# Performance work log

Measured on AMD Instinct MI355X. Metric: run time of the kernel, lower is better.

The kernel has to match this reference:

```python
import jax, jax.numpy as jnp
import numpy as np

B, S, DIM = 2, 2048, 2048
H, KVH, HD = 16, 4, 128
G = H // KVH  # GQA groups = 4
THETA = 10000.0


def setup_inputs() -> dict:
    key = jax.random.key(0)
    k0, k1, k2, k3, k4 = jax.random.split(key, 5)
    x = jax.random.normal(k0, (B, S, DIM), jnp.float32)
    # RoPE table: [max_seq_len, head_dim//2, 2] holding (cos, sin)
    inv_freq = 1.0 / (THETA ** (jnp.arange(0, HD, 2, dtype=jnp.float32) / HD))
    angles = jnp.outer(jnp.arange(S, dtype=jnp.float32), inv_freq)  # [S, HD//2]
    freqs_cis = jnp.stack([jnp.cos(angles), jnp.sin(angles)], axis=-1)
    sc = 0.02
    wq = jax.random.normal(k1, (H * HD, DIM), jnp.float32) * sc
    wk = jax.random.normal(k2, (KVH * HD, DIM), jnp.float32) * sc
    wv = jax.random.normal(k3, (KVH * HD, DIM), jnp.float32) * sc
    wo = jax.random.normal(k4, (DIM, H * HD), jnp.float32) * sc
    return {"x": x, "freqs_cis": freqs_cis, "wq": wq, "wk": wk, "wv": wv, "wo": wo}


def apply_rope(x, freqs_cis):
    # x: [B, S, h, HD]; freqs_cis: [max_S, HD//2, 2]
    s = x.shape[1]
    xr = x.astype(jnp.float32).reshape(*x.shape[:-1], -1, 2)  # [B,S,h,HD//2,2]
    cos = freqs_cis[:s, :, 0][None, :, None, :]  # [1,S,1,HD//2]
    sin = freqs_cis[:s, :, 1][None, :, None, :]
    x0, x1 = xr[..., 0], xr[..., 1]
    out = jnp.stack([x0 * cos - x1 * sin, x0 * sin + x1 * cos], axis=-1)
    return out.reshape(x.shape).astype(x.dtype)


def reference(x, freqs_cis, wq, wk, wv, wo):
    b, s, d = x.shape
    q = (x @ wq.T).reshape(b, s, H, HD)
    k = (x @ wk.T).reshape(b, s, KVH, HD)
    v = (x @ wv.T).reshape(b, s, KVH, HD)
    q = apply_rope(q, freqs_cis)
    k = apply_rope(k, freqs_cis)
    # GQA expand: repeat_interleave along head dim
    k = jnp.repeat(k, G, axis=2)  # [b,s,H,HD]
    v = jnp.repeat(v, G, axis=2)
    q = jnp.swapaxes(q, 1, 2)  # [b,H,s,HD]
    k = jnp.swapaxes(k, 1, 2)
    v = jnp.swapaxes(v, 1, 2)
    scale = 1.0 / jnp.sqrt(jnp.asarray(HD, dtype=q.dtype))
    scores = jnp.einsum('bhqd,bhkd->bhqk', q, k) * scale  # [b,H,s,s]
    causal = jnp.tril(jnp.ones((s, s), dtype=bool))
    scores = jnp.where(causal[None, None], scores, jnp.finfo(scores.dtype).min)
    probs = jax.nn.softmax(scores, axis=-1)
    attn = jnp.einsum('bhqk,bhkd->bhqd', probs, v)  # [b,H,s,HD]
    attn = jnp.swapaxes(attn, 1, 2).reshape(b, s, H * HD)
    return attn @ wo.T
```

## Files before the change

kernel.cpp:

```cpp
#include <hip/hip_runtime.h>
#include <stdint.h>

#define B_ 2
#define S_ 2048
#define DIM_ 2048
#define H_ 16
#define KVH_ 4
#define HD_ 128

typedef short short8 __attribute__((ext_vector_type(8)));
typedef float f4 __attribute__((ext_vector_type(4)));
typedef float f16v __attribute__((ext_vector_type(16)));
typedef unsigned int uint2v __attribute__((ext_vector_type(2)));
typedef unsigned short u16;

#define KSCALE (0.08838834764831845f * 1.4426950408889634f)

__device__ __forceinline__ float bf2f(u16 u) {
    union { unsigned int i; float f; } c; c.i = ((unsigned int)u) << 16; return c.f;
}
__device__ __forceinline__ u16 f2bf(float f) {
    union { float f; unsigned int i; } c; c.f = f;
    return (u16)((c.i + 0x7fffu + ((c.i >> 16) & 1u)) >> 16);
}
__device__ __forceinline__ unsigned pk_bf16(float lo, float hi) {
    unsigned r;
    asm("v_cvt_pk_bf16_f32 %0, %1, %2" : "=v"(r) : "v"(lo), "v"(hi));
    return r;
}

#define GLDS16(gp, lp) \
    __builtin_amdgcn_global_load_lds((const __attribute__((address_space(1))) unsigned int*)(gp), \
                                     (__attribute__((address_space(3))) unsigned int*)(lp), 16, 0, 0)

#define BAR()     asm volatile("s_barrier" ::: "memory")
#define WAITLGKM() asm volatile("s_waitcnt lgkmcnt(0)" ::: "memory")

__global__ void cast_all(const float* __restrict__ x,  const float* __restrict__ wq,
                         const float* __restrict__ wk, const float* __restrict__ wv,
                         const float* __restrict__ wo,
                         u16* __restrict__ xb, u16* __restrict__ wqkvb, u16* __restrict__ wob) {
    int i = blockIdx.x * 256 + threadIdx.x;
    const float4* src; ushort4* dst; int j;
    if (i < 2097152)      { src = (const float4*)x;  dst = (ushort4*)xb;                 j = i; }
    else if (i < 3145728) { src = (const float4*)wq; dst = (ushort4*)wqkvb;              j = i - 2097152; }
    else if (i < 3407872) { src = (const float4*)wk; dst = (ushort4*)wqkvb + 1048576;    j = i - 3145728; }
    else if (i < 3670016) { src = (const float4*)wv; dst = (ushort4*)wqkvb + 1310720;    j = i - 3407872; }
    else                  { src = (const float4*)wo; dst = (ushort4*)wob;                j = i - 3670016; }
    float4 v = src[j];
    ushort4 o;
    o.x = f2bf(v.x); o.y = f2bf(v.y); o.z = f2bf(v.z); o.w = f2bf(v.w);
    dst[j] = o;
}

template<bool OUT_BF16, int NBX>
__global__ __launch_bounds__(512, 2) void gemm256(const u16* __restrict__ A,
                                                  const u16* __restrict__ W,
                                                  void* __restrict__ Cout,
                                                  int M, int N, int K) {
    __shared__ u16 As[2][16384];
    __shared__ u16 Bs[2][16384];
    int t = threadIdx.x, lane = t & 63, w = t >> 6;
    int quad = lane >> 4, l16 = lane & 15, l7 = lane & 7;
    int wm = w >> 2, wn = w & 3;
    int bid = blockIdx.x;
    int xcd = bid & 7, grp = bid >> 3;
    int bx = grp % NBX, by = (grp / NBX) * 8 + xcd;
    size_t m0 = (size_t)by * 256, n0 = (size_t)bx * 256;

    int srow = lane >> 3;
    int sunit = (lane & 7) ^ srow;
    int rR0a = (w >> 2) * 64 + (w & 3) * 8;
    const u16* Ag = A + (m0 + srow) * (size_t)K + sunit * 8;
    const u16* Bg = W + (n0 + srow) * (size_t)K + sunit * 8;

#define STG_A(pl, tk, r0) GLDS16(Ag + ((size_t)((r0) + w * 8)) * K + (tk) * 64, (pl) + ((r0) + w * 8) * 64)
#define STG_B(pl, tk, r0) GLDS16(Bg + ((size_t)((r0) + w * 8)) * K + (tk) * 64, (pl) + ((r0) + w * 8) * 64)
#define STG_BR(pl, tk, bse) GLDS16(Bg + ((size_t)((bse) + rR0a)) * K + (tk) * 64, (pl) + ((bse) + rR0a) * 64)

#define LDA(mh) { \
    _Pragma("unroll") for (int i_ = 0; i_ < 4; i_++) \
    _Pragma("unroll") for (int k_ = 0; k_ < 2; k_++) \
        a[i_][k_] = *(const short8*)&pAc[(wm * 128 + (mh) * 64 + i_ * 16 + l16) * 64 + (((quad + 4 * k_) ^ l7) << 3)]; }
#define LDB(nh) { \
    _Pragma("unroll") for (int j_ = 0; j_ < 2; j_++) \
    _Pragma("unroll") for (int k_ = 0; k_ < 2; k_++) \
        b[j_][k_] = *(const short8*)&pBc[(wn * 64 + (nh) * 32 + j_ * 16 + l16) * 64 + (((quad + 4 * k_) ^ l7) << 3)]; }
#define MFMA_Q(mh, nh) { \
    __builtin_amdgcn_s_setprio(1); \
    _Pragma("unroll") for (int i_ = 0; i_ < 4; i_++) \
    _Pragma("unroll") for (int j_ = 0; j_ < 2; j_++) \
    _Pragma("unroll") for (int k_ = 0; k_ < 2; k_++) \
        acc[(mh) * 4 + i_][(nh) * 2 + j_] = __builtin_amdgcn_mfma_f32_16x16x32_bf16( \
            a[i_][k_], b[j_][k_], acc[(mh) * 4 + i_][(nh) * 2 + j_], 0, 0, 0); \
    __builtin_amdgcn_s_setprio(0); }

    f4 acc[8][4];
    #pragma unroll
    for (int i = 0; i < 8; i++)
        #pragma unroll
        for (int j = 0; j < 4; j++) acc[i][j] = (f4){0.f, 0.f, 0.f, 0.f};

    int NT = K >> 6;

    #pragma unroll
    for (int pt = 0; pt < 2; pt++) {
        u16* pa = &As[pt][0]; u16* pb = &Bs[pt][0];
        #pragma unroll
        for (int r0 = 0; r0 < 256; r0 += 64) { STG_A(pa, pt, r0); STG_B(pb, pt, r0); }
    }
    asm volatile("s_waitcnt vmcnt(0)" ::: "memory");
    BAR();

    short8 a[4][2], b[2][2];
    for (int tt = 0; tt < NT; tt++) {
        int c = tt & 1, nc = c ^ 1;
        u16* pAc = &As[c][0];  u16* pBc = &Bs[c][0];
        u16* pAn = &As[nc][0]; u16* pBn = &Bs[nc][0];
        bool s1 = (tt >= 1) & (tt + 1 < NT);
        bool s2 = (tt + 2 < NT);
        LDA(0); LDB(0);
        if (s1) { STG_A(pAn, tt + 1, 64); STG_A(pAn, tt + 1, 192); }
        BAR(); WAITLGKM(); MFMA_Q(0, 0); BAR();
        LDB(1);
        if (s1) { STG_BR(pBn, tt + 1, 32); STG_BR(pBn, tt + 1, 160); }
        BAR(); WAITLGKM(); MFMA_Q(0, 1); BAR();
        LDA(1); LDB(0);
        if (s2) { STG_A(pAc, tt + 2, 0); STG_A(pAc, tt + 2, 128); }
        BAR(); WAITLGKM(); MFMA_Q(1, 0); BAR();
        if (s2) asm volatile("s_waitcnt vmcnt(2)" ::: "memory");
        else    asm volatile("s_waitcnt vmcnt(0)" ::: "memory");
        LDB(1);
        if (s2) { STG_BR(pBc, tt + 2, 0); STG_BR(pBc, tt + 2, 128); }
        BAR(); WAITLGKM(); MFMA_Q(1, 1); BAR();
    }

    #pragma unroll
    for (int i = 0; i < 8; i++) {
        size_t row = m0 + wm * 128 + i * 16 + quad * 4;
        #pragma unroll
        for (int j = 0; j < 4; j++) {
            size_t col = n0 + wn * 64 + j * 16 + l16;
            #pragma unroll
            for (int r = 0; r < 4; r++) {
                if (OUT_BF16) ((u16*)Cout)[(row + r) * (size_t)N + col] = f2bf(acc[i][j][r]);
                else          ((float*)Cout)[(row + r) * (size_t)N + col] = acc[i][j][r];
            }
        }
    }
#undef STG_A
#undef STG_B
#undef STG_BR
#undef LDA
#undef LDB
#undef MFMA_Q
}

__global__ __launch_bounds__(256) void pack_k(const u16* __restrict__ QKV,
                                              const float* __restrict__ freqs,
                                              u16* __restrict__ Kp) {
    int gid = blockIdx.x * 256 + threadIdx.x;
    int u = gid & 15, row = (gid >> 4) & 63, kt = (gid >> 10) & 31, bk = gid >> 15;
    int b = bk >> 2, kvh = bk & 3;
    int s = kt * 64 + row;
    int d8 = u ^ (row & 7);
    const u16* src = QKV + (size_t)(b * S_ + s) * 3072 + 2048 + kvh * HD_ + d8 * 8;
    short8 v = *(const short8*)src;
    short8 o;
    #pragma unroll
    for (int jp = 0; jp < 4; jp++) {
        float2 cw = ((const float2*)freqs)[s * 64 + d8 * 4 + jp];
        float x0 = bf2f((u16)v[2 * jp]), x1 = bf2f((u16)v[2 * jp + 1]);
        o[2 * jp]     = (short)f2bf(x0 * cw.x - x1 * cw.y);
        o[2 * jp + 1] = (short)f2bf(x0 * cw.y + x1 * cw.x);
    }
    *(short8*)&Kp[(size_t)gid * 8] = o;
}

__global__ __launch_bounds__(256) void pack_v(const u16* __restrict__ QKV, u16* __restrict__ Vp) {
    __shared__ u16 L[64 * 136];
    int bid = blockIdx.x;
    int bk = bid & 7, kt = bid >> 3;
    int b = bk >> 2, kvh = bk & 3;
    int t = threadIdx.x;
    const u16* src = QKV + (size_t)(b * S_ + kt * 64) * 3072 + 2560 + kvh * HD_;
    #pragma unroll
    for (int it = 0; it < 4; it++) {
        int idx = t + it * 256;
        int r = idx >> 4, c = idx & 15;
        *(short8*)&L[r * 136 + c * 8] = *(const short8*)(src + (size_t)r * 3072 + c * 8);
    }
    __syncthreads();
    u16* dst = Vp + (size_t)(bk * 32 + kt) * 8192;
    #pragma unroll
    for (int it = 0; it < 4; it++) {
        int idx = t + it * 256;
        int hd = idx >> 3, u = idx & 7;
        int k0 = (u ^ (hd & 7)) * 8;
        short8 v;
        #pragma unroll
        for (int jj = 0; jj < 8; jj++) v[jj] = (short)L[(k0 + jj) * 136 + hd];
        *(short8*)&dst[(size_t)idx * 8] = v;
    }
}

__global__ __launch_bounds__(256) __attribute__((amdgpu_waves_per_eu(2, 2)))
void attn_kernel(const u16* __restrict__ QKV,
                 const float* __restrict__ freqs,
                 const u16* __restrict__ Kp,
                 const u16* __restrict__ Vp,
                 u16* __restrict__ Ob) {
    __shared__ u16 Ks[2][8192];
    __shared__ u16 Vs[2][8192];
    int bid = blockIdx.x;
    int jj_ = bid & 255, half = bid >> 8;
    int bk = jj_ & 7, qpr = jj_ >> 3;
    int qb = half ? qpr : 63 - qpr;
    int b = bk >> 2, kvh = bk & 3;
    int t = threadIdx.x, lane = t & 63, w = t >> 6;
    int l31 = lane & 31, hi = lane >> 5, l7 = lane & 7;
    int h = kvh * 4 + w;
    int nkt = (qb >> 1) + 1;

    short8 qf[8];
    {
        int s = qb * 32 + l31;
        const u16* qp = QKV + ((size_t)(b * S_ + s)) * 3072 + h * HD_ + hi * 8;
        const float2* fr2 = (const float2*)freqs;
        #pragma unroll
        for (int ds = 0; ds < 8; ds++) {
            short8 v = *(const short8*)(qp + ds * 16);
            short8 o;
            #pragma unroll
            for (int jp = 0; jp < 4; jp++) {
                float2 cs = fr2[s * 64 + ds * 8 + hi * 4 + jp];
                float x0 = bf2f((u16)v[2 * jp]), x1 = bf2f((u16)v[2 * jp + 1]);
                o[2 * jp]     = (short)f2bf((x0 * cs.x - x1 * cs.y) * KSCALE);
                o[2 * jp + 1] = (short)f2bf((x0 * cs.y + x1 * cs.x) * KSCALE);
            }
            qf[ds] = o;
        }
    }

    float m_i = -3e38f, ls = 0.f;
    f16v o4[4];
    #pragma unroll
    for (int i = 0; i < 4; i++)
        #pragma unroll
        for (int r = 0; r < 16; r++) o4[i][r] = 0.f;

    const u16* Kpb = Kp + (size_t)bk * 32 * 8192;
    const u16* Vpb = Vp + (size_t)bk * 32 * 8192;
    int so = w * 2048 + lane * 8;

    {
        const u16* ks = Kpb + so;
        const u16* vs = Vpb + so;
        #pragma unroll
        for (int i = 0; i < 4; i++) {
            GLDS16(ks + i * 512, &Ks[0][w * 2048 + i * 512]);
            GLDS16(vs + i * 512, &Vs[0][w * 2048 + i * 512]);
        }
    }

    for (int kt = 0; kt < nkt; kt++) {
        int buf = kt & 1;
        __syncthreads();
        if (kt + 1 < nkt) {
            int nb = buf ^ 1;
            const u16* ks = Kpb + (size_t)(kt + 1) * 8192 + so;
            const u16* vs = Vpb + (size_t)(kt + 1) * 8192 + so;
            #pragma unroll
            for (int i = 0; i < 4; i++) {
                GLDS16(ks + i * 512, &Ks[nb][w * 2048 + i * 512]);
                GLDS16(vs + i * 512, &Vs[nb][w * 2048 + i * 512]);
            }
        }

        f16v sacc[2];
        #pragma unroll
        for (int k2 = 0; k2 < 2; k2++)
            #pragma unroll
            for (int r = 0; r < 16; r++) sacc[k2][r] = 0.f;
        __builtin_amdgcn_s_setprio(1);
        #pragma unroll
        for (int ds = 0; ds < 8; ds++) {
            int uK = ((ds * 2 + hi) ^ l7) * 8;
            short8 kf0 = *(const short8*)&Ks[buf][l31 * 128 + uK];
            short8 kf1 = *(const short8*)&Ks[buf][(32 + l31) * 128 + uK];
            sacc[0] = __builtin_amdgcn_mfma_f32_32x32x16_bf16(kf0, qf[ds], sacc[0], 0, 0, 0);
            sacc[1] = __builtin_amdgcn_mfma_f32_32x32x16_bf16(kf1, qf[ds], sacc[1], 0, 0, 0);
        }
        __builtin_amdgcn_s_setprio(0);

        short8 vf[16];
        #pragma unroll
        for (int ks = 0; ks < 4; ks++) {
            int uV = ((ks * 2 + hi) ^ l7) * 8;
            #pragma unroll
            for (int ht = 0; ht < 4; ht++)
                vf[ks * 4 + ht] = *(const short8*)&Vs[buf][(ht * 32 + l31) * 64 + uV];
        }

        if (kt == nkt - 1) {
            int off0 = kt * 64 - qb * 32;
            #pragma unroll
            for (int k2 = 0; k2 < 2; k2++) {
                #pragma unroll
                for (int r = 0; r < 16; r++) {
                    int colo = off0 + k2 * 32 + (r & 3) + ((r >> 2) << 3) + (hi << 2);
                    if (colo > l31) sacc[k2][r] = -3e38f;
                }
            }
        }

        float mx[16];
        #pragma unroll
        for (int r = 0; r < 16; r++) mx[r] = fmaxf(sacc[0][r], sacc[1][r]);
        #pragma unroll
        for (int s_ = 8; s_ > 0; s_ >>= 1)
            #pragma unroll
            for (int r = 0; r < s_; r++) mx[r] = fmaxf(mx[r], mx[r + s_]);
        float pm = fmaxf(mx[0], __shfl_xor(mx[0], 32, 64));
        if (__any(pm > m_i + 8.0f)) {
            float mnew = fmaxf(m_i, pm);
            float al = exp2f(m_i - mnew);
            ls *= al;
            #pragma unroll
            for (int i = 0; i < 4; i++)
                #pragma unroll
                for (int r = 0; r < 16; r++) o4[i][r] *= al;
            m_i = mnew;
        }

        short8 pa[4];
        #pragma unroll
        for (int k2 = 0; k2 < 2; k2++) {
            float p[16];
            #pragma unroll
            for (int r = 0; r < 16; r++) p[r] = exp2f(sacc[k2][r] - m_i);
            float s0 = (p[0] + p[1]) + (p[2] + p[3]);
            float s1 = (p[4] + p[5]) + (p[6] + p[7]);
            float s2 = (p[8] + p[9]) + (p[10] + p[11]);
            float s3 = (p[12] + p[13]) + (p[14] + p[15]);
            ls += (s0 + s1) + (s2 + s3);
            unsigned W0 = pk_bf16(p[0], p[1]),   W1 = pk_bf16(p[2], p[3]);
            unsigned W2 = pk_bf16(p[4], p[5]),   W3 = pk_bf16(p[6], p[7]);
            unsigned W4 = pk_bf16(p[8], p[9]),   W5 = pk_bf16(p[10], p[11]);
            unsigned W6 = pk_bf16(p[12], p[13]), W7 = pk_bf16(p[14], p[15]);
            uint2v r02 = __builtin_amdgcn_permlane32_swap(W0, W2, false, false);
            uint2v r13 = __builtin_amdgcn_permlane32_swap(W1, W3, false, false);
            uint2v r46 = __builtin_amdgcn_permlane32_swap(W4, W6, false, false);
            uint2v r57 = __builtin_amdgcn_permlane32_swap(W5, W7, false, false);
            union { unsigned u[4]; short8 s8; } flo, fhi;
            flo.u[0] = r02[0]; flo.u[1] = r13[0]; flo.u[2] = r02[1]; flo.u[3] = r13[1];
            fhi.u[0] = r46[0]; fhi.u[1] = r57[0]; fhi.u[2] = r46[1]; fhi.u[3] = r57[1];
            pa[k2 * 2]     = flo.s8;
            pa[k2 * 2 + 1] = fhi.s8;
        }

        __builtin_amdgcn_s_setprio(1);
        #pragma unroll
        for (int ks = 0; ks < 4; ks++) {
            #pragma unroll
            for (int ht = 0; ht < 4; ht++)
                o4[ht] = __builtin_amdgcn_mfma_f32_32x32x16_bf16(vf[ks * 4 + ht], pa[ks], o4[ht], 0, 0, 0);
        }
        __builtin_amdgcn_s_setprio(0);
    }

    ls += __shfl_xor(ls, 32, 64);
    float rl = 1.0f / ls;
    size_t row = (size_t)b * S_ + qb * 32 + l31;
    u16* op = Ob + row * 2048 + h * HD_;
    #pragma unroll
    for (int ht = 0; ht < 4; ht++) {
        #pragma unroll
        for (int g = 0; g < 4; g++) {
            ushort4 st;
            st.x = f2bf(o4[ht][4 * g + 0] * rl);
            st.y = f2bf(o4[ht][4 * g + 1] * rl);
            st.z = f2bf(o4[ht][4 * g + 2] * rl);
            st.w = f2bf(o4[ht][4 * g + 3] * rl);
            *(ushort4*)&op[ht * 32 + g * 8 + hi * 4] = st;
        }
    }
}

extern "C" void kernel_launch(void* const* d_in, const int* in_sizes, int n_in,
                              void* d_out, int out_size, void* d_ws, size_t ws_size,
                              hipStream_t stream) {
    const float* x     = (const float*)d_in[0];
    const float* freqs = (const float*)d_in[1];
    const float* wq    = (const float*)d_in[2];
    const float* wk    = (const float*)d_in[3];
    const float* wv    = (const float*)d_in[4];
    const float* wo    = (const float*)d_in[5];
    float* out = (float*)d_out;

    char* p = (char*)d_ws;
    u16* xb    = (u16*)p; p += (size_t)4096 * 2048 * 2;
    u16* wqkvb = (u16*)p; p += (size_t)3072 * 2048 * 2;
    u16* wob   = (u16*)p; p += (size_t)2048 * 2048 * 2;
    u16* QKVb  = (u16*)p; p += (size_t)4096 * 3072 * 2;
    u16* Kpb   = (u16*)p; p += (size_t)8 * 32 * 8192 * 2;
    u16* Vpb   = (u16*)p; p += (size_t)8 * 32 * 8192 * 2;
    u16* attnb = xb;

    cast_all<<<18432, 256, 0, stream>>>(x, wq, wk, wv, wo, xb, wqkvb, wob);

    gemm256<true, 12><<<192, 512, 0, stream>>>(xb, wqkvb, QKVb, 4096, 3072, 2048);

    pack_k<<<1024, 256, 0, stream>>>(QKVb, freqs, Kpb);
    pack_v<<<256, 256, 0, stream>>>(QKVb, Vpb);

    attn_kernel<<<512, 256, 0, stream>>>(QKVb, freqs, Kpb, Vpb, attnb);

    gemm256<false, 8><<<128, 512, 0, stream>>>(attnb, wob, out, 4096, 2048, 2048);
}
```

Measured before the change: 318.0 us.

## Pack K/V in MFMA fragment order and load directly from global per-wave

The K and V packing kernels now write tiles in the exact per-lane MFMA fragment order, so the attention kernel can read its operands with contiguous 16-byte global loads instead of staging through LDS. The attention kernel becomes single-wave blocks (2048 blocks of 64 threads), each handling one head and q-block, with a new causal-balanced block ordering. This removes LDS staging, barriers and the double-buffer logic. In exchange it loses the sharing of K/V tiles across the four GQA heads in one block, relies on L2 for reuse, and has no explicit prefetch of the next tile.

Result: no change. 319.9 us (+0.6%).

```diff
diff --git a/kernel.cpp b/kernel.cpp
--- a/kernel.cpp
+++ b/kernel.cpp
@@ -160,16 +160,18 @@
                                               const float* __restrict__ freqs,
                                               u16* __restrict__ Kp) {
     int gid = blockIdx.x * 256 + threadIdx.x;
-    int u = gid & 15, row = (gid >> 4) & 63, kt = (gid >> 10) & 31, bk = gid >> 15;
+    int lane = gid & 63, j = (gid >> 6) & 1, ds = (gid >> 7) & 7;
+    int kt = (gid >> 10) & 31, bk = gid >> 15;
     int b = bk >> 2, kvh = bk & 3;
-    int s = kt * 64 + row;
-    int d8 = u ^ (row & 7);
-    const u16* src = QKV + (size_t)(b * S_ + s) * 3072 + 2048 + kvh * HD_ + d8 * 8;
+    int l31 = lane & 31, hi = lane >> 5;
+    int s = kt * 64 + j * 32 + l31;
+    int d0 = ds * 16 + hi * 8;
+    const u16* src = QKV + (size_t)(b * S_ + s) * 3072 + 2048 + kvh * HD_ + d0;
     short8 v = *(const short8*)src;
     short8 o;
     #pragma unroll
     for (int jp = 0; jp < 4; jp++) {
-        float2 cw = ((const float2*)freqs)[s * 64 + d8 * 4 + jp];
+        float2 cw = ((const float2*)freqs)[s * 64 + ds * 8 + hi * 4 + jp];
         float x0 = bf2f((u16)v[2 * jp]), x1 = bf2f((u16)v[2 * jp + 1]);
         o[2 * jp]     = (short)f2bf(x0 * cw.x - x1 * cw.y);
         o[2 * jp + 1] = (short)f2bf(x0 * cw.y + x1 * cw.x);
@@ -195,8 +197,10 @@
     #pragma unroll
     for (int it = 0; it < 4; it++) {
         int idx = t + it * 256;
-        int hd = idx >> 3, u = idx & 7;
-        int k0 = (u ^ (hd & 7)) * 8;
+        int frag = idx >> 6, lane = idx & 63;
+        int ks = frag >> 2, ht = frag & 3;
+        int hd = ht * 32 + (lane & 31);
+        int k0 = ks * 16 + (lane >> 5) * 8;
         short8 v;
         #pragma unroll
         for (int jj = 0; jj < 8; jj++) v[jj] = (short)L[(k0 + jj) * 136 + hd];
@@ -204,22 +208,21 @@
     }
 }
 
-__global__ __launch_bounds__(256) __attribute__((amdgpu_waves_per_eu(2, 2)))
+__global__ __launch_bounds__(64, 2)
 void attn_kernel(const u16* __restrict__ QKV,
                  const float* __restrict__ freqs,
                  const u16* __restrict__ Kp,
                  const u16* __restrict__ Vp,
                  u16* __restrict__ Ob) {
-    __shared__ u16 Ks[2][8192];
-    __shared__ u16 Vs[2][8192];
     int bid = blockIdx.x;
-    int jj_ = bid & 255, half = bid >> 8;
-    int bk = jj_ & 7, qpr = jj_ >> 3;
-    int qb = half ? qpr : 63 - qpr;
+    int k8 = bid >> 8;
+    int c  = bid & 255;
+    int bk = c & 7, h4 = (c >> 3) & 3, tq = c >> 5;
+    int qb = k8 * 8 + ((k8 & 1) ? 7 - tq : tq);
     int b = bk >> 2, kvh = bk & 3;
-    int t = threadIdx.x, lane = t & 63, w = t >> 6;
-    int l31 = lane & 31, hi = lane >> 5, l7 = lane & 7;
-    int h = kvh * 4 + w;
+    int lane = threadIdx.x;
+    int l31 = lane & 31, hi = lane >> 5;
+    int h = kvh * 4 + h4;
     int nkt = (qb >> 1) + 1;
 
     short8 qf[8];
@@ -251,56 +254,27 @@
 
     const u16* Kpb = Kp + (size_t)bk * 32 * 8192;
     const u16* Vpb = Vp + (size_t)bk * 32 * 8192;
-    int so = w * 2048 + lane * 8;
-
-    {
-        const u16* ks = Kpb + so;
-        const u16* vs = Vpb + so;
-        #pragma unroll
-        for (int i = 0; i < 4; i++) {
-            GLDS16(ks + i * 512, &Ks[0][w * 2048 + i * 512]);
-            GLDS16(vs + i * 512, &Vs[0][w * 2048 + i * 512]);
-        }
-    }
 
     for (int kt = 0; kt < nkt; kt++) {
-        int buf = kt & 1;
-        __syncthreads();
-        if (kt + 1 < nkt) {
-            int nb = buf ^ 1;
-            const u16* ks = Kpb + (size_t)(kt + 1) * 8192 + so;
-            const u16* vs = Vpb + (size_t)(kt + 1) * 8192 + so;
-            #pragma unroll
-            for (int i = 0; i < 4; i++) {
-                GLDS16(ks + i * 512, &Ks[nb][w * 2048 + i * 512]);
-                GLDS16(vs + i * 512, &Vs[nb][w * 2048 + i * 512]);
-            }
-        }
+        const u16* kb = Kpb + (size_t)kt * 8192 + lane * 8;
+        const u16* vb = Vpb + (size_t)kt * 8192 + lane * 8;
 
         f16v sacc[2];
         #pragma unroll
         for (int k2 = 0; k2 < 2; k2++)
             #pragma unroll
             for (int r = 0; r < 16; r++) sacc[k2][r] = 0.f;
-        __builtin_amdgcn_s_setprio(1);
         #pragma unroll
         for (int ds = 0; ds < 8; ds++) {
-            int uK = ((ds * 2 + hi) ^ l7) * 8;
-            short8 kf0 = *(const short8*)&Ks[buf][l31 * 128 + uK];
-            short8 kf1 = *(const short8*)&Ks[buf][(32 + l31) * 128 + uK];
+            short8 kf0 = *(const short8*)(kb + ds * 1024);
+            short8 kf1 = *(const short8*)(kb + ds * 1024 + 512);
             sacc[0] = __builtin_amdgcn_mfma_f32_32x32x16_bf16(kf0, qf[ds], sacc[0], 0, 0, 0);
             sacc[1] = __builtin_amdgcn_mfma_f32_32x32x16_bf16(kf1, qf[ds], sacc[1], 0, 0, 0);
         }
-        __builtin_amdgcn_s_setprio(0);
 
         short8 vf[16];
         #pragma unroll
-        for (int ks = 0; ks < 4; ks++) {
-            int uV = ((ks * 2 + hi) ^ l7) * 8;
-            #pragma unroll
-            for (int ht = 0; ht < 4; ht++)
-                vf[ks * 4 + ht] = *(const short8*)&Vs[buf][(ht * 32 + l31) * 64 + uV];
-        }
+        for (int f = 0; f < 16; f++) vf[f] = *(const short8*)(vb + f * 512);
 
         if (kt == nkt - 1) {
             int off0 = kt * 64 - qb * 32;
@@ -414,7 +388,7 @@
     pack_k<<<1024, 256, 0, stream>>>(QKVb, freqs, Kpb);
     pack_v<<<256, 256, 0, stream>>>(QKVb, Vpb);
 
-    attn_kernel<<<512, 256, 0, stream>>>(QKVb, freqs, Kpb, Vpb, attnb);
+    attn_kernel<<<2048, 64, 0, stream>>>(QKVb, freqs, Kpb, Vpb, attnb);
 
     gemm256<false, 8><<<128, 512, 0, stream>>>(attnb, wob, out, 4096, 2048, 2048);
 }
```
